# Performance work log

Hardware: AMD Instinct MI355X
Metric: run time of the kernel (lower is better)

The kernel has to match this reference:

```python
import jax, jax.numpy as jnp
import numpy as np

K = 7           # kernel_size
GROUPS = 16     # channels // group_channels = 256 // 16
GC = 16         # group_channels
BN_EPS = 1e-5


def setup_inputs() -> dict:
    key = jax.random.key(0)
    ks = jax.random.split(key, 6)
    B, C, H, W = 4, 256, 64, 64
    cr = C // 4                      # reduction_ratio = 4
    k2g = K * K * GROUPS             # conv2 out channels = 784
    return {
        "feature_map": jax.random.normal(ks[0], (B, C, H, W), jnp.float32),
        "guide_map":   jax.random.normal(ks[1], (B, C, H, W), jnp.float32),
        "w1": jax.random.normal(ks[2], (cr, C), jnp.float32) * 0.05,
        "bn_gamma": jnp.ones((cr,), jnp.float32),
        "bn_beta":  jnp.zeros((cr,), jnp.float32),
        "bn_mean":  jax.random.normal(ks[3], (cr,), jnp.float32) * 0.1,
        "bn_var":   jax.random.uniform(ks[4], (cr,), jnp.float32, 0.5, 1.5),
        "w2": jax.random.normal(ks[5], (k2g, cr), jnp.float32) * 0.05,
        "b2": jnp.zeros((k2g,), jnp.float32),
    }


def reference(feature_map, guide_map, w1, bn_gamma, bn_beta, bn_mean, bn_var, w2, b2):
    b, c, h, w = feature_map.shape
    # conv1 (1x1) + BN (inference stats) + ReLU
    x = jnp.einsum("oc,bchw->bohw", w1, guide_map)
    inv = bn_gamma / jnp.sqrt(bn_var + BN_EPS)
    x = x * inv[None, :, None, None] + (bn_beta - bn_mean * inv)[None, :, None, None]
    x = jax.nn.relu(x)
    # conv2 (1x1): dynamic per-pixel kernel weights -> [b, groups, k^2, h, w]
    weight = jnp.einsum("oc,bchw->bohw", w2, x) + b2[None, :, None, None]
    weight = weight.reshape(b, GROUPS, K * K, h, w)
    # unfold feature_map (same padding, stride 1) -> [b, c, k^2, h, w]
    pad = (K - 1) // 2
    fp = jnp.pad(feature_map, ((0, 0), (0, 0), (pad, pad), (pad, pad)))
    patches = jnp.stack(
        [fp[:, :, i:i + h, j:j + w] for i in range(K) for j in range(K)], axis=2
    )
    patches = patches.reshape(b, GROUPS, GC, K * K, h, w)
    # dynamic weighted aggregation over kernel positions, then residual
    out = jnp.einsum("bgkhw,bgckhw->bgchw", weight, patches)
    return out.reshape(b, c, h, w) + feature_map
```

## Files before the change

### kernel.cpp

```cpp
#include <hip/hip_runtime.h>

#define BN_EPS 1e-5f

typedef __bf16 bf16_t;
typedef __bf16 bf16x8 __attribute__((ext_vector_type(8)));
typedef __bf16 bf16x4 __attribute__((ext_vector_type(4)));
typedef __bf16 bf16x2 __attribute__((ext_vector_type(2)));
typedef float  floatx4 __attribute__((ext_vector_type(4)));

#define MFMA16(a, b, c) __builtin_amdgcn_mfma_f32_16x16x32_bf16((a), (b), (c), 0, 0, 0)

#define XT_OFF 0

#define GTP 264

__global__ __launch_bounds__(512) void conv1_k(
    const float* __restrict__ guide, const float* __restrict__ w1,
    const float* __restrict__ gamma, const float* __restrict__ beta,
    const float* __restrict__ mean,  const float* __restrict__ var,
    bf16_t* __restrict__ xT)
{
    __shared__ __attribute__((aligned(16))) bf16_t gTs[64 * GTP];
    const int b = blockIdx.x >> 6, h = blockIdx.x & 63;
    const int t = threadIdx.x;

    const float* gsrc = guide + (size_t)b * 256 * 4096 + h * 64;
#pragma unroll
    for (int i = 0; i < 16; ++i) {
        const int idx = i * 512 + t;
        const int c2 = idx >> 6, p = idx & 63;
        const float g0 = gsrc[(size_t)(2 * c2) * 4096 + p];
        const float g1 = gsrc[(size_t)(2 * c2 + 1) * 4096 + p];
        bf16x2 pk; pk[0] = (bf16_t)g0; pk[1] = (bf16_t)g1;
        *(bf16x2*)&gTs[p * GTP + 2 * c2] = pk;
    }
    __syncthreads();

    const int wv = t >> 6, ln = t & 63, l15 = ln & 15, q = ln >> 4;
    const int ot = wv & 3;
    const int ph = wv >> 2;
    const int o = ot * 16 + l15;
    const float iv = gamma[o] * rsqrtf(var[o] + BN_EPS);

    floatx4 acc[2] = {};
#pragma unroll
    for (int ks = 0; ks < 8; ++ks) {
        const float* wp = w1 + o * 256 + ks * 32 + q * 8;
        const float4 a0 = *(const float4*)(wp);
        const float4 a1 = *(const float4*)(wp + 4);
        bf16x8 a;
        a[0] = (bf16_t)(a0.x * iv); a[1] = (bf16_t)(a0.y * iv);
        a[2] = (bf16_t)(a0.z * iv); a[3] = (bf16_t)(a0.w * iv);
        a[4] = (bf16_t)(a1.x * iv); a[5] = (bf16_t)(a1.y * iv);
        a[6] = (bf16_t)(a1.z * iv); a[7] = (bf16_t)(a1.w * iv);
#pragma unroll
        for (int nt = 0; nt < 2; ++nt) {
            const bf16x8 bb = *(const bf16x8*)&gTs[(ph * 32 + nt * 16 + l15) * GTP + ks * 32 + q * 8];
            acc[nt] = MFMA16(a, bb, acc[nt]);
        }
    }
    float bi[4];
#pragma unroll
    for (int j = 0; j < 4; ++j) {
        const int o2 = ot * 16 + q * 4 + j;
        const float iv2 = gamma[o2] * rsqrtf(var[o2] + BN_EPS);
        bi[j] = beta[o2] - mean[o2] * iv2;
    }
#pragma unroll
    for (int nt = 0; nt < 2; ++nt) {
        const int p = ph * 32 + nt * 16 + l15;
        bf16x4 v;
#pragma unroll
        for (int j = 0; j < 4; ++j) v[j] = (bf16_t)fmaxf(acc[nt][j] + bi[j], 0.f);
        *(bf16x4*)(xT + ((size_t)(b * 64 + h) * 64 + p) * 64 + ot * 16 + q * 4) = v;
    }
}

#define FSR 72
#define FSC 584
#define WGP 136

__global__ __launch_bounds__(256) void fused_k(
    const bf16_t* __restrict__ xT, const float* __restrict__ w2,
    const float* __restrict__ b2,  const float* __restrict__ feat,
    float* __restrict__ out)
{
    __shared__ __attribute__((aligned(16))) float  fs[16 * FSC];
    __shared__ __attribute__((aligned(16))) bf16_t wgs[49 * WGP];

    const int g = blockIdx.x & 15;
    const int rest = blockIdx.x >> 4;
    const int b = rest >> 5, hp = rest & 31;
    const int h0 = hp * 2;
    const int t = threadIdx.x;
    const int wv = t >> 6, ln = t & 63, l15 = ln & 15, q = ln >> 4;

    float4 fsv[9];
    int    fsa[9];
#pragma unroll
    for (int i = 0; i < 9; ++i) {
        const int u = i * 256 + t;
        const int c = u / 144, rem = u - c * 144;
        const int rr = rem / 18, qq = rem - rr * 18;
        const int hh = h0 - 3 + rr;
        float4 v = {0.f, 0.f, 0.f, 0.f};
        if (qq >= 1 && qq <= 16 && hh >= 0 && hh < 64)
            v = *(const float4*)(feat + ((size_t)(b * 256 + g * 16 + c) * 64 + hh) * 64 + (qq - 1) * 4);
        fsv[i] = v;
        fsa[i] = c * FSC + rr * FSR + qq * 4;
    }

    {
        floatx4 acc[4][2] = {};
        const bf16_t* brow = xT + ((size_t)(b * 64 + h0) * 64 + wv * 32) * 64;
#pragma unroll
        for (int ks = 0; ks < 2; ++ks) {
            bf16x8 bfr[2];
            bfr[0] = *(const bf16x8*)(brow + l15 * 64 + ks * 32 + q * 8);
            bfr[1] = *(const bf16x8*)(brow + (16 + l15) * 64 + ks * 32 + q * 8);
#pragma unroll
            for (int mt = 0; mt < 4; ++mt) {
                int row = mt * 16 + l15; if (row > 48) row = 48;
                const float* wp = w2 + (size_t)(g * 49 + row) * 64 + ks * 32 + q * 8;
                const float4 a0 = *(const float4*)(wp);
                const float4 a1 = *(const float4*)(wp + 4);
                bf16x8 a;
                a[0] = (bf16_t)a0.x; a[1] = (bf16_t)a0.y; a[2] = (bf16_t)a0.z; a[3] = (bf16_t)a0.w;
                a[4] = (bf16_t)a1.x; a[5] = (bf16_t)a1.y; a[6] = (bf16_t)a1.z; a[7] = (bf16_t)a1.w;
                acc[mt][0] = MFMA16(a, bfr[0], acc[mt][0]);
                acc[mt][1] = MFMA16(a, bfr[1], acc[mt][1]);
            }
        }
#pragma unroll
        for (int mt = 0; mt < 4; ++mt) {
#pragma unroll
            for (int j = 0; j < 4; ++j) {
                const int k = mt * 16 + q * 4 + j;
                if (k < 49) {
                    const float bias = b2[g * 49 + k];
                    wgs[k * WGP + wv * 32 + l15]      = (bf16_t)(acc[mt][0][j] + bias);
                    wgs[k * WGP + wv * 32 + 16 + l15] = (bf16_t)(acc[mt][1][j] + bias);
                }
            }
        }
    }

#pragma unroll
    for (int i = 0; i < 9; ++i)
        *(float4*)&fs[fsa[i]] = fsv[i];
    __syncthreads();

    const int wq = t & 15, r = (t >> 4) & 1, cp = t >> 5;
    const int w0 = wq * 4;
    const int ch0 = cp * 2;

#define LOAD_STAGE(di, WA, FA, FB) do {                                        \
        const bf16_t* wrow_ = &wgs[((di) * 7) * WGP + r * 64 + w0];            \
        _Pragma("unroll")                                                      \
        for (int dj = 0; dj < 7; ++dj) WA[dj] = *(const bf16x4*)(wrow_ + dj * WGP); \
        const float* p0_ = &fs[ch0 * FSC + ((di) + r) * FSR + w0];             \
        const float* p1_ = p0_ + FSC;                                          \
        _Pragma("unroll")                                                      \
        for (int qj = 0; qj < 3; ++qj) {                                       \
            FA[qj] = *(const floatx4*)(p0_ + qj * 4);                          \
            FB[qj] = *(const floatx4*)(p1_ + qj * 4);                          \
        }                                                                      \
    } while (0)

#define FMA_STAGE(WA, FA, FB) do {                                             \
        _Pragma("unroll")                                                      \
        for (int dj = 0; dj < 7; ++dj) {                                       \
            const bf16x4 wb_ = WA[dj];                                         \
            _Pragma("unroll")                                                  \
            for (int x = 0; x < 4; ++x) {                                      \
                const int e = x + dj + 1;                                      \
                const float wf_ = (float)wb_[x];                               \
                acc[0][x] = fmaf(wf_, FA[e >> 2][e & 3], acc[0][x]);           \
                acc[1][x] = fmaf(wf_, FB[e >> 2][e & 3], acc[1][x]);           \
            }                                                                  \
        }                                                                      \
    } while (0)

    float acc[2][4] = {};
    bf16x4 waA[7], waB[7];
    floatx4 faA[3], fbA[3], faB[3], fbB[3];

    LOAD_STAGE(0, waA, faA, fbA);
    LOAD_STAGE(1, waB, faB, fbB);
    FMA_STAGE(waA, faA, fbA);
    LOAD_STAGE(2, waA, faA, fbA);
    FMA_STAGE(waB, faB, fbB);
    LOAD_STAGE(3, waB, faB, fbB);
    FMA_STAGE(waA, faA, fbA);
    LOAD_STAGE(4, waA, faA, fbA);
    FMA_STAGE(waB, faB, fbB);
    LOAD_STAGE(5, waB, faB, fbB);
    FMA_STAGE(waA, faA, fbA);
    LOAD_STAGE(6, waA, faA, fbA);
    FMA_STAGE(waB, faB, fbB);
    FMA_STAGE(waA, faA, fbA);

#undef LOAD_STAGE
#undef FMA_STAGE

#pragma unroll
    for (int c = 0; c < 2; ++c) {
        const floatx4 res = *(const floatx4*)&fs[(ch0 + c) * FSC + (r + 3) * FSR + 4 + w0];
        const size_t ob = ((size_t)(b * 256 + g * 16 + ch0 + c) * 64 + h0 + r) * 64 + w0;
        float4 o;
        o.x = acc[c][0] + res[0]; o.y = acc[c][1] + res[1];
        o.z = acc[c][2] + res[2]; o.w = acc[c][3] + res[3];
        *(float4*)(out + ob) = o;
    }
}

extern "C" void kernel_launch(void* const* d_in, const int* in_sizes, int n_in,
                              void* d_out, int out_size, void* d_ws, size_t ws_size,
                              hipStream_t stream) {
    const float* feature = (const float*)d_in[0];
    const float* guide   = (const float*)d_in[1];
    const float* w1      = (const float*)d_in[2];
    const float* gamma   = (const float*)d_in[3];
    const float* beta    = (const float*)d_in[4];
    const float* mean    = (const float*)d_in[5];
    const float* var     = (const float*)d_in[6];
    const float* w2      = (const float*)d_in[7];
    const float* b2      = (const float*)d_in[8];
    float* out = (float*)d_out;

    bf16_t* xT = (bf16_t*)((char*)d_ws + XT_OFF);

    conv1_k<<<256, 512, 0, stream>>>(guide, w1, gamma, beta, mean, var, xT);
    fused_k<<<2048, 256, 0, stream>>>(xT, w2, b2, feature, out);
}
```

Measured before the change: 129.0 us.

## Process eight rows per block with double-buffered weights and direct global feature reads

```diff
diff --git a/kernel.cpp b/kernel.cpp
--- a/kernel.cpp
+++ b/kernel.cpp
@@ -76,8 +76,6 @@
     }
 }
 
-#define FSR 72
-#define FSC 584
 #define WGP 136
 
 __global__ __launch_bounds__(256) void fused_k(
@@ -85,32 +83,23 @@
     const float* __restrict__ b2,  const float* __restrict__ feat,
     float* __restrict__ out)
 {
-    __shared__ __attribute__((aligned(16))) float  fs[16 * FSC];
-    __shared__ __attribute__((aligned(16))) bf16_t wgs[49 * WGP];
+    __shared__ __attribute__((aligned(16))) bf16_t wgs[2][49 * WGP];
 
     const int g = blockIdx.x & 15;
     const int rest = blockIdx.x >> 4;
-    const int b = rest >> 5, hp = rest & 31;
-    const int h0 = hp * 2;
+    const int b = rest >> 3, oct = rest & 7;
+    const int hbase = oct * 8;
     const int t = threadIdx.x;
     const int wv = t >> 6, ln = t & 63, l15 = ln & 15, q = ln >> 4;
 
-    float4 fsv[9];
-    int    fsa[9];
-#pragma unroll
-    for (int i = 0; i < 9; ++i) {
-        const int u = i * 256 + t;
-        const int c = u / 144, rem = u - c * 144;
-        const int rr = rem / 18, qq = rem - rr * 18;
-        const int hh = h0 - 3 + rr;
-        float4 v = {0.f, 0.f, 0.f, 0.f};
-        if (qq >= 1 && qq <= 16 && hh >= 0 && hh < 64)
-            v = *(const float4*)(feat + ((size_t)(b * 256 + g * 16 + c) * 64 + hh) * 64 + (qq - 1) * 4);
-        fsv[i] = v;
-        fsa[i] = c * FSC + rr * FSR + qq * 4;
-    }
-
-    {
+    const int wq = t & 15, r = (t >> 4) & 1, cp = t >> 5;
+    const int w0 = wq * 4;
+    const int ch0 = cp * 2;
+    const bool q0v = (w0 > 0);
+    const bool q2v = (w0 < 60);
+    const float* fbase = feat + ((size_t)(b * 256 + g * 16 + ch0) * 64) * 64;
+
+    auto compute_wg = [&](int h0, int buf) {
         floatx4 acc[4][2] = {};
         const bf16_t* brow = xT + ((size_t)(b * 64 + h0) * 64 + wv * 32) * 64;
 #pragma unroll
@@ -138,33 +127,30 @@
                 const int k = mt * 16 + q * 4 + j;
                 if (k < 49) {
                     const float bias = b2[g * 49 + k];
-                    wgs[k * WGP + wv * 32 + l15]      = (bf16_t)(acc[mt][0][j] + bias);
-                    wgs[k * WGP + wv * 32 + 16 + l15] = (bf16_t)(acc[mt][1][j] + bias);
+                    wgs[buf][k * WGP + wv * 32 + l15]      = (bf16_t)(acc[mt][0][j] + bias);
+                    wgs[buf][k * WGP + wv * 32 + 16 + l15] = (bf16_t)(acc[mt][1][j] + bias);
                 }
             }
         }
-    }
-
-#pragma unroll
-    for (int i = 0; i < 9; ++i)
-        *(float4*)&fs[fsa[i]] = fsv[i];
-    __syncthreads();
-
-    const int wq = t & 15, r = (t >> 4) & 1, cp = t >> 5;
-    const int w0 = wq * 4;
-    const int ch0 = cp * 2;
-
+    };
+
+    auto do_agg = [&](int h0, int buf) {
 #define LOAD_STAGE(di, WA, FA, FB) do {                                        \
-        const bf16_t* wrow_ = &wgs[((di) * 7) * WGP + r * 64 + w0];            \
+        const bf16_t* wrow_ = &wgs[buf][((di) * 7) * WGP + r * 64 + w0];       \
         _Pragma("unroll")                                                      \
         for (int dj = 0; dj < 7; ++dj) WA[dj] = *(const bf16x4*)(wrow_ + dj * WGP); \
-        const float* p0_ = &fs[ch0 * FSC + ((di) + r) * FSR + w0];             \
-        const float* p1_ = p0_ + FSC;                                          \
-        _Pragma("unroll")                                                      \
-        for (int qj = 0; qj < 3; ++qj) {                                       \
-            FA[qj] = *(const floatx4*)(p0_ + qj * 4);                          \
-            FB[qj] = *(const floatx4*)(p1_ + qj * 4);                          \
-        }                                                                      \
+        const int hh_ = h0 + r + (di) - 3;                                     \
+        const bool rv_ = (hh_ >= 0) && (hh_ < 64);                             \
+        const float* f0_ = fbase + (ptrdiff_t)hh_ * 64;                        \
+        const float* f1_ = f0_ + 4096;                                         \
+        FA[0] = (floatx4){0.f,0.f,0.f,0.f}; FB[0] = FA[0];                     \
+        FA[1] = FA[0]; FB[1] = FA[0]; FA[2] = FA[0]; FB[2] = FA[0];            \
+        if (rv_ && q0v) { FA[0] = *(const floatx4*)(f0_ + w0 - 4);             \
+                          FB[0] = *(const floatx4*)(f1_ + w0 - 4); }           \
+        if (rv_)        { FA[1] = *(const floatx4*)(f0_ + w0);                 \
+                          FB[1] = *(const floatx4*)(f1_ + w0); }               \
+        if (rv_ && q2v) { FA[2] = *(const floatx4*)(f0_ + w0 + 4);             \
+                          FB[2] = *(const floatx4*)(f1_ + w0 + 4); }           \
     } while (0)
 
 #define FMA_STAGE(WA, FA, FB) do {                                             \
@@ -181,36 +167,49 @@
         }                                                                      \
     } while (0)
 
-    float acc[2][4] = {};
-    bf16x4 waA[7], waB[7];
-    floatx4 faA[3], fbA[3], faB[3], fbB[3];
-
-    LOAD_STAGE(0, waA, faA, fbA);
-    LOAD_STAGE(1, waB, faB, fbB);
-    FMA_STAGE(waA, faA, fbA);
-    LOAD_STAGE(2, waA, faA, fbA);
-    FMA_STAGE(waB, faB, fbB);
-    LOAD_STAGE(3, waB, faB, fbB);
-    FMA_STAGE(waA, faA, fbA);
-    LOAD_STAGE(4, waA, faA, fbA);
-    FMA_STAGE(waB, faB, fbB);
-    LOAD_STAGE(5, waB, faB, fbB);
-    FMA_STAGE(waA, faA, fbA);
-    LOAD_STAGE(6, waA, faA, fbA);
-    FMA_STAGE(waB, faB, fbB);
-    FMA_STAGE(waA, faA, fbA);
+        float acc[2][4] = {};
+        bf16x4 waA[7], waB[7];
+        floatx4 faA[3], fbA[3], faB[3], fbB[3];
+
+        LOAD_STAGE(0, waA, faA, fbA);
+        LOAD_STAGE(1, waB, faB, fbB);
+        FMA_STAGE(waA, faA, fbA);
+        LOAD_STAGE(2, waA, faA, fbA);
+        FMA_STAGE(waB, faB, fbB);
+        LOAD_STAGE(3, waB, faB, fbB);
+        FMA_STAGE(waA, faA, fbA);
+        LOAD_STAGE(4, waA, faA, fbA);
+        FMA_STAGE(waB, faB, fbB);
+        LOAD_STAGE(5, waB, faB, fbB);
+        FMA_STAGE(waA, faA, fbA);
+        LOAD_STAGE(6, waA, faA, fbA);
+        FMA_STAGE(waB, faB, fbB);
+        FMA_STAGE(waA, faA, fbA);
 
 #undef LOAD_STAGE
 #undef FMA_STAGE
 
 #pragma unroll
-    for (int c = 0; c < 2; ++c) {
-        const floatx4 res = *(const floatx4*)&fs[(ch0 + c) * FSC + (r + 3) * FSR + 4 + w0];
-        const size_t ob = ((size_t)(b * 256 + g * 16 + ch0 + c) * 64 + h0 + r) * 64 + w0;
-        float4 o;
-        o.x = acc[c][0] + res[0]; o.y = acc[c][1] + res[1];
-        o.z = acc[c][2] + res[2]; o.w = acc[c][3] + res[3];
-        *(float4*)(out + ob) = o;
+        for (int c = 0; c < 2; ++c) {
+            const floatx4 res = *(const floatx4*)(fbase + (size_t)c * 4096 + (h0 + r) * 64 + w0);
+            const size_t ob = ((size_t)(b * 256 + g * 16 + ch0 + c) * 64 + h0 + r) * 64 + w0;
+            float4 o;
+            o.x = acc[c][0] + res[0]; o.y = acc[c][1] + res[1];
+            o.z = acc[c][2] + res[2]; o.w = acc[c][3] + res[3];
+            *(float4*)(out + ob) = o;
+        }
+    };
+
+    compute_wg(hbase, 0);
+    __syncthreads();
+#pragma unroll
+    for (int p = 0; p < 4; ++p) {
+        const int h0 = hbase + p * 2;
+        do_agg(h0, p & 1);
+        if (p < 3) {
+            compute_wg(h0 + 2, (p + 1) & 1);
+            __syncthreads();
+        }
     }
 }
 
@@ -231,5 +230,5 @@
     bf16_t* xT = (bf16_t*)((char*)d_ws + XT_OFF);
 
     conv1_k<<<256, 512, 0, stream>>>(guide, w1, gamma, beta, mean, var, xT);
-    fused_k<<<2048, 256, 0, stream>>>(xT, w2, b2, feature, out);
+    fused_k<<<512, 256, 0, stream>>>(xT, w2, b2, feature, out);
 }
```

Measured after the change: 141.7 us. 1.1x slower.
